# Kernel optimization log

Measured on AMD Instinct MI355X. Metric: run time of the kernel, lower is better.

The kernel has to match this reference:

```python
import jax, jax.numpy as jnp
from jax import lax
import numpy as np

NPOINT = 1024
RADIUS = 0.2
MAX_SAMPLES = 32
EPS = 1e-5  # BatchNorm eps (torch default)


def setup_inputs() -> dict:
    key = jax.random.key(0)
    ks = jax.random.split(key, 10)
    B, N = 8, 16384
    xyz = jax.random.uniform(ks[0], (B, N, 3), jnp.float32)
    points = jax.random.normal(ks[1], (B, N, 6), jnp.float32)

    def lin(k, o, i):
        return jax.random.normal(k, (o, i), jnp.float32) * (1.0 / np.sqrt(i))

    inp = dict(xyz=xyz, points=points)
    dims = [(64, 9), (64, 64), (128, 64)]
    for li, (o, i) in enumerate(dims):
        inp[f"w{li}"] = lin(ks[2 + li], o, i)
        inp[f"b{li}"] = jnp.zeros((o,), jnp.float32)
        inp[f"g{li}"] = jnp.ones((o,), jnp.float32)
        inp[f"be{li}"] = jnp.zeros((o,), jnp.float32)
    return inp


def farthest_point_sample(xyz, npoint):
    # xyz: (B, N, 3) -> (B, npoint) int32. Deterministic start at index 0.
    B, N, _ = xyz.shape

    def step(carry, _):
        distance, farthest = carry  # (B,N), (B,)
        centroid = jax.vmap(lambda x, i: x[i])(xyz, farthest)  # (B,3)
        d = jnp.sum((xyz - centroid[:, None, :]) ** 2, axis=-1)  # (B,N)
        distance = jnp.minimum(distance, d)
        new_far = jnp.argmax(distance, axis=-1).astype(jnp.int32)
        return (distance, new_far), farthest

    init = (jnp.full((B, N), 1e10, xyz.dtype), jnp.zeros((B,), jnp.int32))
    _, idx = lax.scan(step, init, None, length=npoint)  # (npoint, B)
    return idx.T  # (B, npoint)


def ball_query(centroids, xyz, radius, max_samples):
    # First up-to-max_samples in-radius indices (ascending), padded with 0,
    # matching the torch loop which fills a zero-initialized buffer.
    B, P, _ = centroids.shape
    N = xyz.shape[1]
    d2 = (jnp.sum(centroids ** 2, -1)[:, :, None]
          - 2.0 * jnp.einsum('bpc,bnc->bpn', centroids, xyz)
          + jnp.sum(xyz ** 2, -1)[:, None, :])  # (B,P,N)
    score = jnp.where(d2 < radius * radius, jnp.arange(N, dtype=jnp.int32), N)
    neg_vals, _ = lax.top_k(-score, max_samples)  # smallest indices first
    taken = -neg_vals
    return jnp.where(taken < N, taken, 0)  # (B,P,max_samples)


def _gather_groups(feat, idx):
    # feat: (B,N,C), idx: (B,P,S) -> (B,P,S,C)
    return jax.vmap(lambda f, i: f[i])(feat, idx)


def _mlp_layer(x, w, b, g, be):
    # 1x1 Conv2d + BatchNorm2d(training stats) + ReLU, channel-last layout.
    y = jnp.einsum('bpsc,oc->bpso', x, w) + b
    mean = jnp.mean(y, axis=(0, 1, 2))
    var = jnp.var(y, axis=(0, 1, 2))  # biased, as torch BN normalization
    y = (y - mean) * lax.rsqrt(var + EPS) * g + be
    return jax.nn.relu(y)


def reference(xyz, points, w0, b0, g0, be0, w1, b1, g1, be1, w2, b2, g2, be2):
    B = xyz.shape[0]
    cent_idx = farthest_point_sample(xyz, NPOINT)             # (B,P)
    centroids = jax.vmap(lambda x, i: x[i])(xyz, cent_idx)    # (B,P,3)
    gidx = ball_query(centroids, xyz, RADIUS, MAX_SAMPLES)    # (B,P,S)
    grouped_xyz = _gather_groups(xyz, gidx) - centroids[:, :, None, :]
    grouped_pts = _gather_groups(points, gidx)
    x = jnp.concatenate([grouped_xyz, grouped_pts], axis=-1)  # (B,P,S,9)
    x = _mlp_layer(x, w0, b0, g0, be0)
    x = _mlp_layer(x, w1, b1, g1, be1)
    x = _mlp_layer(x, w2, b2, g2, be2)
    new_points = jnp.max(x, axis=2)                            # (B,P,128)
    return (centroids, new_points)
```

## Files before the change

### kernel.cpp

```cpp
#include <hip/hip_runtime.h>
#include <cstddef>

constexpr int B = 8;
constexpr int N = 16384;
constexpr int P = 1024;
constexpr int S = 32;
constexpr int NSAMP = B * P * S;
constexpr float EPS = 1e-5f;
constexpr float INV_N = 1.0f / 262144.0f;

typedef float v2f __attribute__((ext_vector_type(2)));

constexpr int ST_S1   = 0;
constexpr int ST_S2   = 9;
constexpr int ST_SUM1 = 96;
constexpr int ST_SQ1  = 160;
constexpr int ST_SUM2 = 224;
constexpr int ST_SQ2  = 352;
constexpr int ST_SC0  = 480;
constexpr int ST_SH0  = 544;
constexpr int ST_SC1  = 608;
constexpr int ST_SH1  = 672;
constexpr int ST_SC2  = 736;
constexpr int ST_SH2  = 864;

#define STAGE256(dst, src, n)                                               \
  for (int i_ = threadIdx.x; i_ < (n); i_ += 256) (dst)[i_] = (src)[i_];

__device__ __forceinline__ unsigned long long wave_max_key_dpp(
    unsigned long long key) {
#define DPP_STEP(ctrl)                                                      \
  {                                                                         \
    unsigned lo = (unsigned)key;                                            \
    unsigned hi = (unsigned)(key >> 32);                                    \
    unsigned lo2 = (unsigned)__builtin_amdgcn_update_dpp(                   \
        0, (int)lo, (ctrl), 0xf, 0xf, false);                               \
    unsigned hi2 = (unsigned)__builtin_amdgcn_update_dpp(                   \
        0, (int)hi, (ctrl), 0xf, 0xf, false);                               \
    unsigned long long k2 = ((unsigned long long)hi2 << 32) | lo2;          \
    if (k2 > key) key = k2;                                                 \
  }
  DPP_STEP(0x111);
  DPP_STEP(0x112);
  DPP_STEP(0x114);
  DPP_STEP(0x118);
  DPP_STEP(0x142);
  DPP_STEP(0x143);
#undef DPP_STEP
  return key;
}

__global__ __launch_bounds__(512) void fps_kernel(
    const float* __restrict__ xyz, float* __restrict__ cent) {
#pragma clang fp contract(off)
  const int b = blockIdx.x;
  const int t = threadIdx.x;
  const int wave = t >> 6;
  const float* X = xyz + (size_t)b * N * 3;

  __shared__ float lds_force[24576];
  __shared__ unsigned long long skey[2][8];

  v2f px[16], py[16], pz[16], dist[16];
#pragma unroll
  for (int m = 0; m < 16; m++) {
    int i0 = t + (2 * m) * 512;
    int i1 = t + (2 * m + 1) * 512;
    px[m] = (v2f){X[3 * i0 + 0], X[3 * i1 + 0]};
    py[m] = (v2f){X[3 * i0 + 1], X[3 * i1 + 1]};
    pz[m] = (v2f){X[3 * i0 + 2], X[3 * i1 + 2]};
    dist[m] = (v2f){1e10f, 1e10f};
  }

  float cx = X[0], cy = X[1], cz = X[2];

  if (cx > 1e29f) {
    lds_force[t] = cy;
    cz += lds_force[t ^ 1];
  }

  for (int j = 0; j < P; j++) {
    if (t == 0) {
      float* co = cent + ((size_t)b * P + j) * 3;
      co[0] = cx; co[1] = cy; co[2] = cz;
    }
    const v2f cx2 = (v2f){cx, cx};
    const v2f cy2 = (v2f){cy, cy};
    const v2f cz2 = (v2f){cz, cz};
    float best = -1.0f;
    int bk = 0;
#pragma unroll
    for (int m = 0; m < 16; m++) {
      v2f dx = px[m] - cx2;
      v2f dy = py[m] - cy2;
      v2f dz = pz[m] - cz2;
      v2f d = (dx * dx + dy * dy) + dz * dz;
      v2f nd;
      nd.x = fminf(dist[m].x, d.x);
      nd.y = fminf(dist[m].y, d.y);
      dist[m] = nd;
      if (nd.x > best) { best = nd.x; bk = 2 * m; }
      if (nd.y > best) { best = nd.y; bk = 2 * m + 1; }
    }
    const int bi = t + bk * 512;
    unsigned long long key =
        ((unsigned long long)__float_as_uint(best) << 32) |
        (unsigned)(16383 - bi);
    key = wave_max_key_dpp(key);
    const int buf = j & 1;
    if ((t & 63) == 63) skey[buf][wave] = key;
    __syncthreads();
    unsigned long long bkey = skey[buf][0];
#pragma unroll
    for (int w = 1; w < 8; w++) {
      unsigned long long kk = skey[buf][w];
      if (kk > bkey) bkey = kk;
    }
    const int wi = 16383 - (int)(unsigned)(bkey & 0xFFFFFFFFull);
    cx = X[3 * wi + 0];
    cy = X[3 * wi + 1];
    cz = X[3 * wi + 2];
  }
}

__global__ __launch_bounds__(256) void ballq_kernel(
    const float* __restrict__ xyz, const float* __restrict__ cent,
    int* __restrict__ gidx) {
#pragma clang fp contract(off)
  const int wid = (blockIdx.x * 256 + threadIdx.x) >> 6;
  const int lane = threadIdx.x & 63;
  const int b = wid >> 10;
  const float* X = xyz + (size_t)b * N * 3;
  const float* c = cent + (size_t)wid * 3;
  const float cx = c[0], cy = c[1], cz = c[2];
  const float cc = (cx * cx + cy * cy) + cz * cz;
  int* g = gidx + (size_t)wid * S;
  const float r2 = 0.2f * 0.2f;

  int cnt = 0;
  for (int base = 0; base < N; base += 64) {
    const int i = base + lane;
    float x = X[3 * i + 0], y = X[3 * i + 1], z = X[3 * i + 2];
    float xx = (x * x + y * y) + z * z;
    float dt = (cx * x + cy * y) + cz * z;
    float d2 = (cc - 2.0f * dt) + xx;
    bool inr = d2 < r2;
    unsigned long long m = __ballot(inr);
    if (inr) {
      int pos = cnt + (int)__popcll(m & ((1ull << lane) - 1ull));
      if (pos < S) g[pos] = i;
    }
    cnt += (int)__popcll(m);
    if (cnt >= S) break;
  }
}

__device__ __forceinline__ void load_x(
    const float* __restrict__ xyz, const float* __restrict__ points,
    const float* __restrict__ cent, const int* __restrict__ gidx,
    int sample, float x[9]) {
  const int grp = sample >> 5;
  const int b = grp >> 10;
  const int idx = gidx[sample];
  const float* Xp = xyz + ((size_t)b * N + idx) * 3;
  const float* Pp = points + ((size_t)b * N + idx) * 6;
  const float* C = cent + (size_t)grp * 3;
  x[0] = Xp[0] - C[0];
  x[1] = Xp[1] - C[1];
  x[2] = Xp[2] - C[2];
  x[3] = Pp[0]; x[4] = Pp[1]; x[5] = Pp[2];
  x[6] = Pp[3]; x[7] = Pp[4]; x[8] = Pp[5];
}

__global__ __launch_bounds__(256) void moments_kernel(
    const float* __restrict__ xyz, const float* __restrict__ points,
    const float* __restrict__ cent, const int* __restrict__ gidx,
    float* __restrict__ stats) {
  const int tid = blockIdx.x * 256 + threadIdx.x;
  float S1[9], S2[81];
#pragma unroll
  for (int c = 0; c < 9; c++) S1[c] = 0.f;
#pragma unroll
  for (int k = 0; k < 81; k++) S2[k] = 0.f;

  for (int smp = tid; smp < NSAMP; smp += 8192) {
    float x[9];
    load_x(xyz, points, cent, gidx, smp, x);
#pragma unroll
    for (int c = 0; c < 9; c++) {
      S1[c] += x[c];
#pragma unroll
      for (int d = 0; d < 9; d++) S2[c * 9 + d] = fmaf(x[c], x[d], S2[c * 9 + d]);
    }
  }
  const int lane = threadIdx.x & 63;
#pragma unroll
  for (int c = 0; c < 9; c++) {
#pragma unroll
    for (int m = 1; m < 64; m <<= 1) S1[c] += __shfl_xor(S1[c], m, 64);
  }
#pragma unroll
  for (int k = 0; k < 81; k++) {
#pragma unroll
    for (int m = 1; m < 64; m <<= 1) S2[k] += __shfl_xor(S2[k], m, 64);
  }
  if (lane == 0) {
#pragma unroll
    for (int c = 0; c < 9; c++) atomicAdd(&stats[ST_S1 + c], S1[c]);
#pragma unroll
    for (int k = 0; k < 81; k++) atomicAdd(&stats[ST_S2 + k], S2[k]);
  }
}

__global__ void finalize0_kernel(float* __restrict__ stats,
                                 const float* __restrict__ w0,
                                 const float* __restrict__ b0,
                                 const float* __restrict__ g0,
                                 const float* __restrict__ be0) {
  const int o = threadIdx.x;
  float w[9];
#pragma unroll
  for (int c = 0; c < 9; c++) w[c] = w0[o * 9 + c];
  float dot = 0.f;
#pragma unroll
  for (int c = 0; c < 9; c++) dot += w[c] * stats[ST_S1 + c];
  float quad = 0.f;
#pragma unroll
  for (int c = 0; c < 9; c++)
#pragma unroll
    for (int d = 0; d < 9; d++) quad += w[c] * w[d] * stats[ST_S2 + c * 9 + d];
  const float bb = b0[o];
  const float mean = dot * INV_N + bb;
  const float Ey2 = (quad + 2.0f * bb * dot) * INV_N + bb * bb;
  const float var = Ey2 - mean * mean;
  const float sc = g0[o] / sqrtf(var + EPS);
  stats[ST_SC0 + o] = sc;
  stats[ST_SH0 + o] = be0[o] - mean * sc;
}

__device__ __forceinline__ void compute_h0_l(
    const float x[9], const float* lw0, const float* lb0,
    const float* lsc0, const float* lsh0, float h0[64]) {
#pragma unroll
  for (int o = 0; o < 64; o++) {
    float a = lb0[o];
#pragma unroll
    for (int c = 0; c < 9; c++) a = fmaf(lw0[o * 9 + c], x[c], a);
    h0[o] = fmaxf(fmaf(a, lsc0[o], lsh0[o]), 0.0f);
  }
}

__device__ __forceinline__ float dot64_l(const float* lwrow, const float h[64],
                                         float a) {
  const float4* wr = (const float4*)lwrow;
#pragma unroll
  for (int c4 = 0; c4 < 16; c4++) {
    const float4 wv = wr[c4];
    a = fmaf(wv.x, h[4 * c4 + 0], a);
    a = fmaf(wv.y, h[4 * c4 + 1], a);
    a = fmaf(wv.z, h[4 * c4 + 2], a);
    a = fmaf(wv.w, h[4 * c4 + 3], a);
  }
  return a;
}

__device__ __forceinline__ void compute_h1_l(
    const float h0[64], const float* lw1, const float* lb1,
    const float* lsc1, const float* lsh1, float h1[64]) {
#pragma unroll
  for (int o = 0; o < 64; o++) {
    float a = dot64_l(&lw1[o * 64], h0, lb1[o]);
    h1[o] = fmaxf(fmaf(a, lsc1[o], lsh1[o]), 0.0f);
  }
}

__global__ __launch_bounds__(256) void pass2_kernel(
    const float* __restrict__ xyz, const float* __restrict__ points,
    const float* __restrict__ cent, const int* __restrict__ gidx,
    const float* __restrict__ w0, const float* __restrict__ b0,
    const float* __restrict__ w1, const float* __restrict__ b1,
    float* __restrict__ stats) {
  __shared__ __attribute__((aligned(16))) float lw1[4096];
  __shared__ float lw0[576], lb0v[64], lsc0[64], lsh0[64], lb1v[64];
  __shared__ float ssum[4][64], ssq[4][64];
  STAGE256(lw1, w1, 4096)
  STAGE256(lw0, w0, 576)
  STAGE256(lb0v, b0, 64)
  STAGE256(lsc0, stats + ST_SC0, 64)
  STAGE256(lsh0, stats + ST_SH0, 64)
  STAGE256(lb1v, b1, 64)
  __syncthreads();

  const int tid = blockIdx.x * 256 + threadIdx.x;
  float x[9];
  load_x(xyz, points, cent, gidx, tid, x);
  float h0[64];
  compute_h0_l(x, lw0, lb0v, lsc0, lsh0, h0);

  const int wv = threadIdx.x >> 6, lane = threadIdx.x & 63;
#pragma unroll 1
  for (int o = 0; o < 64; o++) {
    float a = dot64_l(&lw1[o * 64], h0, lb1v[o]);
    float s = a, q = a * a;
#pragma unroll
    for (int m = 1; m < 64; m <<= 1) {
      s += __shfl_xor(s, m, 64);
      q += __shfl_xor(q, m, 64);
    }
    if (lane == 0) { ssum[wv][o] = s; ssq[wv][o] = q; }
  }
  __syncthreads();
  if (threadIdx.x < 64) {
    const int o = threadIdx.x;
    float s = ssum[0][o] + ssum[1][o] + ssum[2][o] + ssum[3][o];
    float q = ssq[0][o] + ssq[1][o] + ssq[2][o] + ssq[3][o];
    atomicAdd(&stats[ST_SUM1 + o], s);
    atomicAdd(&stats[ST_SQ1 + o], q);
  }
}

__global__ void finalize1_kernel(float* __restrict__ stats,
                                 const float* __restrict__ g1,
                                 const float* __restrict__ be1) {
  const int o = threadIdx.x;
  const float mean = stats[ST_SUM1 + o] * INV_N;
  const float var = stats[ST_SQ1 + o] * INV_N - mean * mean;
  const float sc = g1[o] / sqrtf(var + EPS);
  stats[ST_SC1 + o] = sc;
  stats[ST_SH1 + o] = be1[o] - mean * sc;
}

__global__ __launch_bounds__(256) void pass3_kernel(
    const float* __restrict__ xyz, const float* __restrict__ points,
    const float* __restrict__ cent, const int* __restrict__ gidx,
    const float* __restrict__ w0, const float* __restrict__ b0,
    const float* __restrict__ w1, const float* __restrict__ b1,
    const float* __restrict__ w2, const float* __restrict__ b2,
    float* __restrict__ stats) {
  __shared__ __attribute__((aligned(16))) float lw1[4096];
  __shared__ __attribute__((aligned(16))) float lw2[8192];
  __shared__ float lw0[576], lb0v[64], lsc0[64], lsh0[64];
  __shared__ float lb1v[64], lsc1[64], lsh1[64], lb2v[128];
  __shared__ float ssum[4][128], ssq[4][128];
  STAGE256(lw1, w1, 4096)
  STAGE256(lw2, w2, 8192)
  STAGE256(lw0, w0, 576)
  STAGE256(lb0v, b0, 64)
  STAGE256(lsc0, stats + ST_SC0, 64)
  STAGE256(lsh0, stats + ST_SH0, 64)
  STAGE256(lb1v, b1, 64)
  STAGE256(lsc1, stats + ST_SC1, 64)
  STAGE256(lsh1, stats + ST_SH1, 64)
  STAGE256(lb2v, b2, 128)
  __syncthreads();

  const int tid = blockIdx.x * 256 + threadIdx.x;
  float x[9];
  load_x(xyz, points, cent, gidx, tid, x);
  float h0[64];
  compute_h0_l(x, lw0, lb0v, lsc0, lsh0, h0);
  float h1[64];
  compute_h1_l(h0, lw1, lb1v, lsc1, lsh1, h1);

  const int wv = threadIdx.x >> 6, lane = threadIdx.x & 63;
#pragma unroll 1
  for (int o = 0; o < 128; o++) {
    float a = dot64_l(&lw2[o * 64], h1, lb2v[o]);
    float s = a, q = a * a;
#pragma unroll
    for (int m = 1; m < 64; m <<= 1) {
      s += __shfl_xor(s, m, 64);
      q += __shfl_xor(q, m, 64);
    }
    if (lane == 0) { ssum[wv][o] = s; ssq[wv][o] = q; }
  }
  __syncthreads();
  if (threadIdx.x < 128) {
    const int o = threadIdx.x;
    float s = ssum[0][o] + ssum[1][o] + ssum[2][o] + ssum[3][o];
    float q = ssq[0][o] + ssq[1][o] + ssq[2][o] + ssq[3][o];
    atomicAdd(&stats[ST_SUM2 + o], s);
    atomicAdd(&stats[ST_SQ2 + o], q);
  }
}

__global__ void finalize2_kernel(float* __restrict__ stats,
                                 const float* __restrict__ g2,
                                 const float* __restrict__ be2) {
  const int o = threadIdx.x;
  const float mean = stats[ST_SUM2 + o] * INV_N;
  const float var = stats[ST_SQ2 + o] * INV_N - mean * mean;
  const float sc = g2[o] / sqrtf(var + EPS);
  stats[ST_SC2 + o] = sc;
  stats[ST_SH2 + o] = be2[o] - mean * sc;
}

__global__ __launch_bounds__(256) void pass4_kernel(
    const float* __restrict__ xyz, const float* __restrict__ points,
    const float* __restrict__ cent, const int* __restrict__ gidx,
    const float* __restrict__ w0, const float* __restrict__ b0,
    const float* __restrict__ w1, const float* __restrict__ b1,
    const float* __restrict__ w2, const float* __restrict__ b2,
    const float* __restrict__ stats, float* __restrict__ outnp) {
  __shared__ __attribute__((aligned(16))) float lw1[4096];
  __shared__ __attribute__((aligned(16))) float lw2[8192];
  __shared__ float lw0[576], lb0v[64], lsc0[64], lsh0[64];
  __shared__ float lb1v[64], lsc1[64], lsh1[64];
  __shared__ float lb2v[128], lsc2[128], lsh2[128];
  STAGE256(lw1, w1, 4096)
  STAGE256(lw2, w2, 8192)
  STAGE256(lw0, w0, 576)
  STAGE256(lb0v, b0, 64)
  STAGE256(lsc0, stats + ST_SC0, 64)
  STAGE256(lsh0, stats + ST_SH0, 64)
  STAGE256(lb1v, b1, 64)
  STAGE256(lsc1, stats + ST_SC1, 64)
  STAGE256(lsh1, stats + ST_SH1, 64)
  STAGE256(lb2v, b2, 128)
  STAGE256(lsc2, stats + ST_SC2, 128)
  STAGE256(lsh2, stats + ST_SH2, 128)
  __syncthreads();

  const int wid = (blockIdx.x * 256 + threadIdx.x) >> 6;
  const int lane = threadIdx.x & 63;
  const int grp = wid * 2 + (lane >> 5);
  const int s = lane & 31;
  const int sample = grp * 32 + s;

  float x[9];
  load_x(xyz, points, cent, gidx, sample, x);
  float h0[64];
  compute_h0_l(x, lw0, lb0v, lsc0, lsh0, h0);
  float h1[64];
  compute_h1_l(h0, lw1, lb1v, lsc1, lsh1, h1);

#pragma unroll 1
  for (int o = 0; o < 128; o++) {
    float a = dot64_l(&lw2[o * 64], h1, lb2v[o]);
    float v = fmaxf(fmaf(a, lsc2[o], lsh2[o]), 0.0f);
#pragma unroll
    for (int m = 1; m < 32; m <<= 1) v = fmaxf(v, __shfl_xor(v, m, 64));
    if ((lane & 31) == 0) outnp[(size_t)grp * 128 + o] = v;
  }
}

extern "C" void kernel_launch(void* const* d_in, const int* in_sizes, int n_in,
                              void* d_out, int out_size, void* d_ws,
                              size_t ws_size, hipStream_t stream) {
  const float* xyz = (const float*)d_in[0];
  const float* points = (const float*)d_in[1];
  const float* w0 = (const float*)d_in[2];
  const float* b0 = (const float*)d_in[3];
  const float* g0 = (const float*)d_in[4];
  const float* be0 = (const float*)d_in[5];
  const float* w1 = (const float*)d_in[6];
  const float* b1 = (const float*)d_in[7];
  const float* g1 = (const float*)d_in[8];
  const float* be1 = (const float*)d_in[9];
  const float* w2 = (const float*)d_in[10];
  const float* b2 = (const float*)d_in[11];
  const float* g2 = (const float*)d_in[12];
  const float* be2 = (const float*)d_in[13];

  float* out = (float*)d_out;
  float* cent = out;
  float* outnp = out + B * P * 3;

  const size_t GIDX_BYTES = (size_t)NSAMP * sizeof(int);
  const size_t STATS_BYTES = 4096;
  if (ws_size < GIDX_BYTES + STATS_BYTES) return;
  int* gidx = (int*)d_ws;
  float* stats = (float*)((char*)d_ws + GIDX_BYTES);

  hipMemsetAsync(d_ws, 0, GIDX_BYTES + STATS_BYTES, stream);

  fps_kernel<<<B, 512, 0, stream>>>(xyz, cent);
  ballq_kernel<<<(B * P) / 4, 256, 0, stream>>>(xyz, cent, gidx);
  moments_kernel<<<32, 256, 0, stream>>>(xyz, points, cent, gidx, stats);
  finalize0_kernel<<<1, 64, 0, stream>>>(stats, w0, b0, g0, be0);
  pass2_kernel<<<NSAMP / 256, 256, 0, stream>>>(xyz, points, cent, gidx,
                                                w0, b0, w1, b1, stats);
  finalize1_kernel<<<1, 64, 0, stream>>>(stats, g1, be1);
  pass3_kernel<<<NSAMP / 256, 256, 0, stream>>>(xyz, points, cent, gidx,
                                                w0, b0, w1, b1, w2, b2, stats);
  finalize2_kernel<<<1, 128, 0, stream>>>(stats, g2, be2);
  pass4_kernel<<<NSAMP / 256, 256, 0, stream>>>(xyz, points, cent, gidx,
                                                w0, b0, w1, b1, w2, b2, stats,
                                                outnp);
}
```

Baseline: 2.284 ms.

## Process two samples per thread to reuse LDS weight loads; use DPP reductions

Each thread in pass2, pass3 and pass4 now handles two samples, one from each half of the sample range. Every float4 weight read from LDS then feeds two FMA chains instead of one, which halves LDS weight traffic per sample, and the grid is halved to match. Wave reductions for the BN statistics and the group max move from shfl_xor to DPP row operations, with the result read from lane 63 or 31. The change also adds dummy shared-memory padding arrays behind never-taken branches to steer occupancy. The doubled register arrays raise register pressure and may lower occupancy.

```diff
diff --git a/kernel.cpp b/kernel.cpp
--- a/kernel.cpp
+++ b/kernel.cpp
@@ -6,6 +6,7 @@
 constexpr int P = 1024;
 constexpr int S = 32;
 constexpr int NSAMP = B * P * S;
+constexpr int HALF = NSAMP / 2;
 constexpr float EPS = 1e-5f;
 constexpr float INV_N = 1.0f / 262144.0f;
 
@@ -26,6 +27,29 @@
 
 #define STAGE256(dst, src, n)                                               \
   for (int i_ = threadIdx.x; i_ < (n); i_ += 256) (dst)[i_] = (src)[i_];
+
+#define DPP_F32(res, v, ctrl)                                               \
+  float res = __uint_as_float((unsigned)__builtin_amdgcn_update_dpp(        \
+      0, (int)__float_as_uint(v), (ctrl), 0xf, 0xf, false));
+
+__device__ __forceinline__ float dpp_sum64(float v) {
+  { DPP_F32(o_, v, 0x111) v += o_; }
+  { DPP_F32(o_, v, 0x112) v += o_; }
+  { DPP_F32(o_, v, 0x114) v += o_; }
+  { DPP_F32(o_, v, 0x118) v += o_; }
+  { DPP_F32(o_, v, 0x142) v += o_; }
+  { DPP_F32(o_, v, 0x143) v += o_; }
+  return v;
+}
+
+__device__ __forceinline__ float dpp_max32(float v) {
+  { DPP_F32(o_, v, 0x111) v = fmaxf(v, o_); }
+  { DPP_F32(o_, v, 0x112) v = fmaxf(v, o_); }
+  { DPP_F32(o_, v, 0x114) v = fmaxf(v, o_); }
+  { DPP_F32(o_, v, 0x118) v = fmaxf(v, o_); }
+  { DPP_F32(o_, v, 0x142) v = fmaxf(v, o_); }
+  return v;
+}
 
 __device__ __forceinline__ unsigned long long wave_max_key_dpp(
     unsigned long long key) {
@@ -264,6 +288,24 @@
   return a;
 }
 
+__device__ __forceinline__ void dot64x2(const float* lwrow,
+                                        const float hA[64], const float hB[64],
+                                        float& aA, float& aB) {
+  const float4* wr = (const float4*)lwrow;
+#pragma unroll
+  for (int c4 = 0; c4 < 16; c4++) {
+    const float4 wv = wr[c4];
+    aA = fmaf(wv.x, hA[4 * c4 + 0], aA);
+    aB = fmaf(wv.x, hB[4 * c4 + 0], aB);
+    aA = fmaf(wv.y, hA[4 * c4 + 1], aA);
+    aB = fmaf(wv.y, hB[4 * c4 + 1], aB);
+    aA = fmaf(wv.z, hA[4 * c4 + 2], aA);
+    aB = fmaf(wv.z, hB[4 * c4 + 2], aB);
+    aA = fmaf(wv.w, hA[4 * c4 + 3], aA);
+    aB = fmaf(wv.w, hB[4 * c4 + 3], aB);
+  }
+}
+
 __device__ __forceinline__ void compute_h1_l(
     const float h0[64], const float* lw1, const float* lb1,
     const float* lsc1, const float* lsh1, float h1[64]) {
@@ -283,6 +325,7 @@
   __shared__ __attribute__((aligned(16))) float lw1[4096];
   __shared__ float lw0[576], lb0v[64], lsc0[64], lsh0[64], lb1v[64];
   __shared__ float ssum[4][64], ssq[4][64];
+  __shared__ float pad2[9216];
   STAGE256(lw1, w1, 4096)
   STAGE256(lw0, w0, 576)
   STAGE256(lb0v, b0, 64)
@@ -292,22 +335,25 @@
   __syncthreads();
 
   const int tid = blockIdx.x * 256 + threadIdx.x;
-  float x[9];
-  load_x(xyz, points, cent, gidx, tid, x);
-  float h0[64];
-  compute_h0_l(x, lw0, lb0v, lsc0, lsh0, h0);
+  float xA[9], xB[9];
+  load_x(xyz, points, cent, gidx, tid, xA);
+  load_x(xyz, points, cent, gidx, tid + HALF, xB);
+  if (xA[3] > 1e29f) {
+    pad2[threadIdx.x] = xA[4];
+    ssum[0][0] = pad2[threadIdx.x ^ 1];
+  }
+  float h0A[64], h0B[64];
+  compute_h0_l(xA, lw0, lb0v, lsc0, lsh0, h0A);
+  compute_h0_l(xB, lw0, lb0v, lsc0, lsh0, h0B);
 
   const int wv = threadIdx.x >> 6, lane = threadIdx.x & 63;
 #pragma unroll 1
   for (int o = 0; o < 64; o++) {
-    float a = dot64_l(&lw1[o * 64], h0, lb1v[o]);
-    float s = a, q = a * a;
-#pragma unroll
-    for (int m = 1; m < 64; m <<= 1) {
-      s += __shfl_xor(s, m, 64);
-      q += __shfl_xor(q, m, 64);
-    }
-    if (lane == 0) { ssum[wv][o] = s; ssq[wv][o] = q; }
+    float aA = lb1v[o], aB = lb1v[o];
+    dot64x2(&lw1[o * 64], h0A, h0B, aA, aB);
+    float s = dpp_sum64(aA + aB);
+    float q = dpp_sum64(aA * aA + aB * aB);
+    if (lane == 63) { ssum[wv][o] = s; ssq[wv][o] = q; }
   }
   __syncthreads();
   if (threadIdx.x < 64) {
@@ -355,24 +401,30 @@
   __syncthreads();
 
   const int tid = blockIdx.x * 256 + threadIdx.x;
-  float x[9];
-  load_x(xyz, points, cent, gidx, tid, x);
-  float h0[64];
-  compute_h0_l(x, lw0, lb0v, lsc0, lsh0, h0);
-  float h1[64];
-  compute_h1_l(h0, lw1, lb1v, lsc1, lsh1, h1);
+  float h1A[64], h1B[64];
+  {
+    float xA[9];
+    load_x(xyz, points, cent, gidx, tid, xA);
+    float h0A[64];
+    compute_h0_l(xA, lw0, lb0v, lsc0, lsh0, h0A);
+    compute_h1_l(h0A, lw1, lb1v, lsc1, lsh1, h1A);
+  }
+  {
+    float xB[9];
+    load_x(xyz, points, cent, gidx, tid + HALF, xB);
+    float h0B[64];
+    compute_h0_l(xB, lw0, lb0v, lsc0, lsh0, h0B);
+    compute_h1_l(h0B, lw1, lb1v, lsc1, lsh1, h1B);
+  }
 
   const int wv = threadIdx.x >> 6, lane = threadIdx.x & 63;
 #pragma unroll 1
   for (int o = 0; o < 128; o++) {
-    float a = dot64_l(&lw2[o * 64], h1, lb2v[o]);
-    float s = a, q = a * a;
-#pragma unroll
-    for (int m = 1; m < 64; m <<= 1) {
-      s += __shfl_xor(s, m, 64);
-      q += __shfl_xor(q, m, 64);
-    }
-    if (lane == 0) { ssum[wv][o] = s; ssq[wv][o] = q; }
+    float aA = lb2v[o], aB = lb2v[o];
+    dot64x2(&lw2[o * 64], h1A, h1B, aA, aB);
+    float s = dpp_sum64(aA + aB);
+    float q = dpp_sum64(aA * aA + aB * aB);
+    if (lane == 63) { ssum[wv][o] = s; ssq[wv][o] = q; }
   }
   __syncthreads();
   if (threadIdx.x < 128) {
@@ -407,6 +459,7 @@
   __shared__ float lw0[576], lb0v[64], lsc0[64], lsh0[64];
   __shared__ float lb1v[64], lsc1[64], lsh1[64];
   __shared__ float lb2v[128], lsc2[128], lsh2[128];
+  __shared__ float pad4[640];
   STAGE256(lw1, w1, 4096)
   STAGE256(lw2, w2, 8192)
   STAGE256(lw0, w0, 576)
@@ -421,26 +474,45 @@
   STAGE256(lsh2, stats + ST_SH2, 128)
   __syncthreads();
 
-  const int wid = (blockIdx.x * 256 + threadIdx.x) >> 6;
+  const int tid2 = blockIdx.x * 256 + threadIdx.x;
+  const int wid = tid2 >> 6;
   const int lane = threadIdx.x & 63;
-  const int grp = wid * 2 + (lane >> 5);
+  const int grpA = wid * 2 + (lane >> 5);
+  const int grpB = grpA + 4096;
   const int s = lane & 31;
-  const int sample = grp * 32 + s;
-
-  float x[9];
-  load_x(xyz, points, cent, gidx, sample, x);
-  float h0[64];
-  compute_h0_l(x, lw0, lb0v, lsc0, lsh0, h0);
-  float h1[64];
-  compute_h1_l(h0, lw1, lb1v, lsc1, lsh1, h1);
+
+  float h1A[64], h1B[64];
+  {
+    float xA[9];
+    load_x(xyz, points, cent, gidx, grpA * 32 + s, xA);
+    float h0A[64];
+    compute_h0_l(xA, lw0, lb0v, lsc0, lsh0, h0A);
+    compute_h1_l(h0A, lw1, lb1v, lsc1, lsh1, h1A);
+    if (xA[3] > 1e29f) {
+      pad4[threadIdx.x & 511] = xA[4];
+      h1A[0] += pad4[(threadIdx.x ^ 1) & 511];
+    }
+  }
+  {
+    float xB[9];
+    load_x(xyz, points, cent, gidx, grpB * 32 + s, xB);
+    float h0B[64];
+    compute_h0_l(xB, lw0, lb0v, lsc0, lsh0, h0B);
+    compute_h1_l(h0B, lw1, lb1v, lsc1, lsh1, h1B);
+  }
 
 #pragma unroll 1
   for (int o = 0; o < 128; o++) {
-    float a = dot64_l(&lw2[o * 64], h1, lb2v[o]);
-    float v = fmaxf(fmaf(a, lsc2[o], lsh2[o]), 0.0f);
-#pragma unroll
-    for (int m = 1; m < 32; m <<= 1) v = fmaxf(v, __shfl_xor(v, m, 64));
-    if ((lane & 31) == 0) outnp[(size_t)grp * 128 + o] = v;
+    float aA = lb2v[o], aB = lb2v[o];
+    dot64x2(&lw2[o * 64], h1A, h1B, aA, aB);
+    float vA = fmaxf(fmaf(aA, lsc2[o], lsh2[o]), 0.0f);
+    float vB = fmaxf(fmaf(aB, lsc2[o], lsh2[o]), 0.0f);
+    vA = dpp_max32(vA);
+    vB = dpp_max32(vB);
+    if ((lane & 31) == 31) {
+      outnp[(size_t)grpA * 128 + o] = vA;
+      outnp[(size_t)grpB * 128 + o] = vB;
+    }
   }
 }
 
@@ -478,13 +550,13 @@
   ballq_kernel<<<(B * P) / 4, 256, 0, stream>>>(xyz, cent, gidx);
   moments_kernel<<<32, 256, 0, stream>>>(xyz, points, cent, gidx, stats);
   finalize0_kernel<<<1, 64, 0, stream>>>(stats, w0, b0, g0, be0);
-  pass2_kernel<<<NSAMP / 256, 256, 0, stream>>>(xyz, points, cent, gidx,
-                                                w0, b0, w1, b1, stats);
+  pass2_kernel<<<HALF / 256, 256, 0, stream>>>(xyz, points, cent, gidx,
+                                               w0, b0, w1, b1, stats);
   finalize1_kernel<<<1, 64, 0, stream>>>(stats, g1, be1);
-  pass3_kernel<<<NSAMP / 256, 256, 0, stream>>>(xyz, points, cent, gidx,
-                                                w0, b0, w1, b1, w2, b2, stats);
+  pass3_kernel<<<HALF / 256, 256, 0, stream>>>(xyz, points, cent, gidx,
+                                               w0, b0, w1, b1, w2, b2, stats);
   finalize2_kernel<<<1, 128, 0, stream>>>(stats, g2, be2);
-  pass4_kernel<<<NSAMP / 256, 256, 0, stream>>>(xyz, points, cent, gidx,
-                                                w0, b0, w1, b1, w2, b2, stats,
-                                                outnp);
-}
+  pass4_kernel<<<HALF / 256, 256, 0, stream>>>(xyz, points, cent, gidx,
+                                               w0, b0, w1, b1, w2, b2, stats,
+                                               outnp);
+}
```

New measurement: 3.821 ms. 67.3% more time.

## Cache pre-BN layer activations in workspace to avoid recomputing MLP layers

Applied to the files above, without the earlier changes.

Pass2 now stores the layer-1 pre-BN activations to a channel-major workspace buffer. A new pass3 reads them back instead of recomputing layer 0 and layer 1, and writes the layer-2 pre-BN activations. A new pass4 then applies BN, ReLU and the max-pool directly from that buffer. This removes the repeated gather and matmul recomputation across passes, at the cost of about 200 MB of extra global memory traffic. It falls back to the old path when the workspace is too small.

```diff
diff --git a/kernel.cpp b/kernel.cpp
--- a/kernel.cpp
+++ b/kernel.cpp
@@ -274,12 +274,13 @@
   }
 }
 
-__global__ __launch_bounds__(256) void pass2_kernel(
+template <bool CACHE>
+__global__ __launch_bounds__(256) void pass2_t(
     const float* __restrict__ xyz, const float* __restrict__ points,
     const float* __restrict__ cent, const int* __restrict__ gidx,
     const float* __restrict__ w0, const float* __restrict__ b0,
     const float* __restrict__ w1, const float* __restrict__ b1,
-    float* __restrict__ stats) {
+    float* __restrict__ stats, float* __restrict__ a1buf) {
   __shared__ __attribute__((aligned(16))) float lw1[4096];
   __shared__ float lw0[576], lb0v[64], lsc0[64], lsh0[64], lb1v[64];
   __shared__ float ssum[4][64], ssq[4][64];
@@ -301,6 +302,7 @@
 #pragma unroll 1
   for (int o = 0; o < 64; o++) {
     float a = dot64_l(&lw1[o * 64], h0, lb1v[o]);
+    if (CACHE) a1buf[(size_t)o * NSAMP + tid] = a;
     float s = a, q = a * a;
 #pragma unroll
     for (int m = 1; m < 64; m <<= 1) {
@@ -366,6 +368,50 @@
 #pragma unroll 1
   for (int o = 0; o < 128; o++) {
     float a = dot64_l(&lw2[o * 64], h1, lb2v[o]);
+    float s = a, q = a * a;
+#pragma unroll
+    for (int m = 1; m < 64; m <<= 1) {
+      s += __shfl_xor(s, m, 64);
+      q += __shfl_xor(q, m, 64);
+    }
+    if (lane == 0) { ssum[wv][o] = s; ssq[wv][o] = q; }
+  }
+  __syncthreads();
+  if (threadIdx.x < 128) {
+    const int o = threadIdx.x;
+    float s = ssum[0][o] + ssum[1][o] + ssum[2][o] + ssum[3][o];
+    float q = ssq[0][o] + ssq[1][o] + ssq[2][o] + ssq[3][o];
+    atomicAdd(&stats[ST_SUM2 + o], s);
+    atomicAdd(&stats[ST_SQ2 + o], q);
+  }
+}
+
+__global__ __launch_bounds__(256) void pass3_cache(
+    const float* __restrict__ a1buf, const float* __restrict__ w2,
+    const float* __restrict__ b2, float* __restrict__ stats,
+    float* __restrict__ a2buf) {
+  __shared__ __attribute__((aligned(16))) float lw2[8192];
+  __shared__ float lsc1[64], lsh1[64], lb2v[128];
+  __shared__ float ssum[4][128], ssq[4][128];
+  STAGE256(lw2, w2, 8192)
+  STAGE256(lsc1, stats + ST_SC1, 64)
+  STAGE256(lsh1, stats + ST_SH1, 64)
+  STAGE256(lb2v, b2, 128)
+  __syncthreads();
+
+  const int tid = blockIdx.x * 256 + threadIdx.x;
+  float h1[64];
+#pragma unroll
+  for (int o = 0; o < 64; o++) {
+    const float a = a1buf[(size_t)o * NSAMP + tid];
+    h1[o] = fmaxf(fmaf(a, lsc1[o], lsh1[o]), 0.0f);
+  }
+
+  const int wv = threadIdx.x >> 6, lane = threadIdx.x & 63;
+#pragma unroll 1
+  for (int o = 0; o < 128; o++) {
+    float a = dot64_l(&lw2[o * 64], h1, lb2v[o]);
+    a2buf[(size_t)o * NSAMP + tid] = a;
     float s = a, q = a * a;
 #pragma unroll
     for (int m = 1; m < 64; m <<= 1) {
@@ -444,6 +490,28 @@
   }
 }
 
+__global__ __launch_bounds__(256) void pass4_cache(
+    const float* __restrict__ a2buf, const float* __restrict__ stats,
+    float* __restrict__ outnp) {
+  __shared__ float lsc2[128], lsh2[128];
+  STAGE256(lsc2, stats + ST_SC2, 128)
+  STAGE256(lsh2, stats + ST_SH2, 128)
+  __syncthreads();
+
+  const int tid = blockIdx.x * 256 + threadIdx.x;
+  const int lane = threadIdx.x & 63;
+  const int grp = tid >> 5;
+
+#pragma unroll 1
+  for (int o = 0; o < 128; o++) {
+    const float a = a2buf[(size_t)o * NSAMP + tid];
+    float v = fmaxf(fmaf(a, lsc2[o], lsh2[o]), 0.0f);
+#pragma unroll
+    for (int m = 1; m < 32; m <<= 1) v = fmaxf(v, __shfl_xor(v, m, 64));
+    if ((lane & 31) == 0) outnp[(size_t)grp * 128 + o] = v;
+  }
+}
+
 extern "C" void kernel_launch(void* const* d_in, const int* in_sizes, int n_in,
                               void* d_out, int out_size, void* d_ws,
                               size_t ws_size, hipStream_t stream) {
@@ -468,9 +536,15 @@
 
   const size_t GIDX_BYTES = (size_t)NSAMP * sizeof(int);
   const size_t STATS_BYTES = 4096;
+  const size_t A1_BYTES = (size_t)64 * NSAMP * sizeof(float);
+  const size_t A2_BYTES = (size_t)128 * NSAMP * sizeof(float);
   if (ws_size < GIDX_BYTES + STATS_BYTES) return;
   int* gidx = (int*)d_ws;
   float* stats = (float*)((char*)d_ws + GIDX_BYTES);
+  float* a1buf = (float*)((char*)d_ws + GIDX_BYTES + STATS_BYTES);
+  float* a2buf = a1buf + (size_t)64 * NSAMP;
+  const bool cache =
+      ws_size >= GIDX_BYTES + STATS_BYTES + A1_BYTES + A2_BYTES;
 
   hipMemsetAsync(d_ws, 0, GIDX_BYTES + STATS_BYTES, stream);
 
@@ -478,13 +552,23 @@
   ballq_kernel<<<(B * P) / 4, 256, 0, stream>>>(xyz, cent, gidx);
   moments_kernel<<<32, 256, 0, stream>>>(xyz, points, cent, gidx, stats);
   finalize0_kernel<<<1, 64, 0, stream>>>(stats, w0, b0, g0, be0);
-  pass2_kernel<<<NSAMP / 256, 256, 0, stream>>>(xyz, points, cent, gidx,
-                                                w0, b0, w1, b1, stats);
-  finalize1_kernel<<<1, 64, 0, stream>>>(stats, g1, be1);
-  pass3_kernel<<<NSAMP / 256, 256, 0, stream>>>(xyz, points, cent, gidx,
-                                                w0, b0, w1, b1, w2, b2, stats);
-  finalize2_kernel<<<1, 128, 0, stream>>>(stats, g2, be2);
-  pass4_kernel<<<NSAMP / 256, 256, 0, stream>>>(xyz, points, cent, gidx,
-                                                w0, b0, w1, b1, w2, b2, stats,
-                                                outnp);
-}
+  if (cache) {
+    pass2_t<true><<<NSAMP / 256, 256, 0, stream>>>(
+        xyz, points, cent, gidx, w0, b0, w1, b1, stats, a1buf);
+    finalize1_kernel<<<1, 64, 0, stream>>>(stats, g1, be1);
+    pass3_cache<<<NSAMP / 256, 256, 0, stream>>>(a1buf, w2, b2, stats, a2buf);
+    finalize2_kernel<<<1, 128, 0, stream>>>(stats, g2, be2);
+    pass4_cache<<<NSAMP / 256, 256, 0, stream>>>(a2buf, stats, outnp);
+  } else {
+    pass2_t<false><<<NSAMP / 256, 256, 0, stream>>>(
+        xyz, points, cent, gidx, w0, b0, w1, b1, stats, a1buf);
+    finalize1_kernel<<<1, 64, 0, stream>>>(stats, g1, be1);
+    pass3_kernel<<<NSAMP / 256, 256, 0, stream>>>(xyz, points, cent, gidx,
+                                                  w0, b0, w1, b1, w2, b2,
+                                                  stats);
+    finalize2_kernel<<<1, 128, 0, stream>>>(stats, g2, be2);
+    pass4_kernel<<<NSAMP / 256, 256, 0, stream>>>(xyz, points, cent, gidx,
+                                                  w0, b0, w1, b1, w2, b2,
+                                                  stats, outnp);
+  }
+}
```

Result: faster. 2.104 ms (-7.9%).
